# Kernel optimization log

Hardware: AMD Instinct MI355X
Metric: run time of the kernel (lower is better)

## Reference

```python
import jax, jax.numpy as jnp
import numpy as np

B, S, D, H = 2, 2048, 1024, 8
DH = D // H          # hidden_dim == attn_dim == 128
TOTAL = 4 * D        # (2*hidden_dim + 2*attn_dim) * H
EPS = 1e-5
ROPE_BASE = 10000.0


def _layernorm(x, g, b):
    m = jnp.mean(x, axis=-1, keepdims=True)
    v = jnp.mean(jnp.square(x - m), axis=-1, keepdims=True)
    return (x - m) * jax.lax.rsqrt(v + EPS) * g + b


def _rope(x):
    # x: [B, H, S, DH], interleaved even/odd RoPE as in the torch module
    half = DH // 2
    inv_freq = 1.0 / (ROPE_BASE ** (jnp.arange(0, DH, 2, dtype=jnp.float32) / DH))  # [half]
    t = jnp.arange(x.shape[2], dtype=jnp.float32)
    freqs = t[:, None] * inv_freq[None, :]                 # [S, half]
    cos = jnp.cos(freqs)[None, None, :, :]                 # [1,1,S,half]
    sin = jnp.sin(freqs)[None, None, :, :]
    xe, xo = x[..., 0::2], x[..., 1::2]
    re = xe * cos - xo * sin
    ro = xe * sin + xo * cos
    return jnp.stack([re, ro], axis=-1).reshape(x.shape)


def setup_inputs() -> dict:
    key = jax.random.key(0)
    ks = jax.random.split(key, 6)
    x = jax.random.normal(ks[0], (B, S, D), dtype=jnp.float32)
    attention_mask = jnp.ones((B, S), dtype=bool)
    # weights stored [in, out] so forward is x @ W + b
    w_uvqk = 0.02 * jax.random.normal(ks[1], (D, TOTAL), dtype=jnp.float32)
    b_uvqk = jnp.zeros((TOTAL,), dtype=jnp.float32)
    w_out = 0.02 * jax.random.normal(ks[2], (3 * D, D), dtype=jnp.float32)
    b_out = jnp.zeros((D,), dtype=jnp.float32)
    ln1_g = jnp.ones((D,), dtype=jnp.float32)
    ln1_b = jnp.zeros((D,), dtype=jnp.float32)
    ln2_g = jnp.ones((D,), dtype=jnp.float32)
    ln2_b = jnp.zeros((D,), dtype=jnp.float32)
    return {"x": x, "attention_mask": attention_mask,
            "ln1_g": ln1_g, "ln1_b": ln1_b,
            "w_uvqk": w_uvqk, "b_uvqk": b_uvqk,
            "ln2_g": ln2_g, "ln2_b": ln2_b,
            "w_out": w_out, "b_out": b_out}


def reference(x, attention_mask, ln1_g, ln1_b, w_uvqk, b_uvqk, ln2_g, ln2_b, w_out, b_out):
    normed = _layernorm(x, ln1_g, ln1_b)
    uvqk = jax.nn.silu(normed @ w_uvqk + b_uvqk)          # [B,S,4D]
    u, v, q, k = jnp.split(uvqk, [D, 2 * D, 3 * D], axis=-1)
    q = q.reshape(B, S, H, DH).transpose(0, 2, 1, 3)      # [B,H,S,DH]
    k = k.reshape(B, S, H, DH).transpose(0, 2, 1, 3)
    v = v.reshape(B, S, H, DH).transpose(0, 2, 1, 3)
    q, k = _rope(q), _rope(k)
    scale = jnp.float32(DH) ** 0.5
    scores = jnp.einsum('bhsd,bhtd->bhst', q, k) / scale  # [B,H,S,S] fp32
    causal = jnp.tril(jnp.ones((S, S), dtype=bool))
    pad = attention_mask[:, None, :, None] & attention_mask[:, None, None, :]
    valid = pad & causal[None, None, :, :]
    scores = jnp.where(valid, scores, jnp.float32(-30.0))
    scores = jnp.clip(scores, -30.0, 30.0)
    attn = jax.nn.silu(scores)                            # SiLU instead of softmax
    ao = jnp.einsum('bhst,bhtd->bhsd', attn, v)           # [B,H,S,DH]
    ao = ao.transpose(0, 2, 1, 3).reshape(B, S, D)
    normed_attn = _layernorm(ao, ln2_g, ln2_b)
    cat = jnp.concatenate([u, ao, normed_attn * u], axis=-1)  # [B,S,3D]
    return x + (cat @ w_out + b_out)
```

## Files before the change

kernel.cpp:

```cpp
#include <hip/hip_runtime.h>
#include <hip/hip_bf16.h>
#include <math.h>

#define Bm 2
#define Sm 2048
#define Dm 1024
#define Hm 8
#define DHm 128
#define TOTALm 4096
#define ROWS (Bm*Sm)
#define K2m (3*Dm)

typedef __bf16 bf16;
typedef __bf16 bf16x8 __attribute__((ext_vector_type(8)));
typedef __bf16 bf16x4 __attribute__((ext_vector_type(4)));
typedef float  f32x4  __attribute__((ext_vector_type(4)));

__device__ __forceinline__ void stage_tile_128x32(
    const bf16* __restrict__ g, int ld, bf16* lds, int tid)
{
    int wid = tid >> 6;
    #pragma unroll
    for (int j = 0; j < 2; j++) {
        int e0  = (j*256 + tid) * 8;
        int row = e0 >> 5, col = e0 & 31;
        const bf16* src = g + (size_t)row*ld + col;
        bf16* dst = lds + (size_t)(j*256 + wid*64)*8;
        __builtin_amdgcn_global_load_lds(
            (const __attribute__((address_space(1))) unsigned int*)src,
            (__attribute__((address_space(3))) unsigned int*)dst,
            16, 0, 0);
    }
}

__device__ __forceinline__ void stage_tile_64x32(
    const bf16* __restrict__ g, int ld, bf16* lds, int tid)
{
    int wid = tid >> 6;
    int e0 = tid * 8;
    int row = e0 >> 5, col = e0 & 31;
    const bf16* src = g + (size_t)row*ld + col;
    bf16* dst = lds + (size_t)wid*512;
    __builtin_amdgcn_global_load_lds(
        (const __attribute__((address_space(1))) unsigned int*)src,
        (__attribute__((address_space(3))) unsigned int*)dst,
        16, 0, 0);
}

__global__ __launch_bounds__(256) void prep_kernel(
    const float* __restrict__ x, const float* __restrict__ g1,
    const float* __restrict__ b1, bf16* __restrict__ normed,
    const float* __restrict__ w_uvqk, bf16* __restrict__ Wt1,
    const float* __restrict__ w_out,  bf16* __restrict__ Wt2,
    float* __restrict__ ct, float* __restrict__ st)
{
    __shared__ float tile[32][33];
    __shared__ float red[4];
    __shared__ float stats[2];
    int bid = blockIdx.x;
    int tid = threadIdx.x;
    if (bid < 7168) {
        const float* in; bf16* out; int R, C, bx, by;
        if (bid < 4096) { in = w_uvqk; out = Wt1; R = Dm;  C = TOTALm; bx = bid & 127; by = bid >> 7; }
        else { int id2 = bid - 4096; in = w_out; out = Wt2; R = K2m; C = Dm; bx = id2 & 31; by = id2 >> 5; }
        int c0 = bx*32, r0 = by*32;
        int tx = tid & 31, ty = tid >> 5;
        for (int i=0;i<4;i++) {
            int r = ty + i*8;
            tile[r][tx] = in[(size_t)(r0+r)*C + c0+tx];
        }
        __syncthreads();
        for (int i=0;i<4;i++) {
            int cl = ty + i*8;
            out[(size_t)(c0+cl)*R + r0+tx] = (bf16)tile[tx][cl];
        }
    } else if (bid < 7680) {
        int idx = (bid - 7168)*256 + tid;
        int t = idx >> 6, p = idx & 63;
        float inv = expf(-0.143911568f * (float)p);
        float f = (float)t * inv;
        float sv, cv;
        sincosf(f, &sv, &cv);
        ct[idx] = cv; st[idx] = sv;
    } else {
        int row = bid - 7680;
        const float* xr = x + (size_t)row * Dm;
        float4 v = *(const float4*)(xr + tid*4);
        float s = v.x+v.y+v.z+v.w;
        for (int o=32;o>0;o>>=1) s += __shfl_down(s,o);
        int wid = tid>>6, lane = tid&63;
        if (lane==0) red[wid]=s;
        __syncthreads();
        if (tid==0) stats[0] = (red[0]+red[1]+red[2]+red[3]) * (1.f/Dm);
        __syncthreads();
        float m = stats[0];
        float d0=v.x-m,d1=v.y-m,d2=v.z-m,d3=v.w-m;
        float q = d0*d0+d1*d1+d2*d2+d3*d3;
        for (int o=32;o>0;o>>=1) q += __shfl_down(q,o);
        if (lane==0) red[wid]=q;
        __syncthreads();
        if (tid==0) stats[1] = rsqrtf((red[0]+red[1]+red[2]+red[3])*(1.f/Dm) + 1e-5f);
        __syncthreads();
        float rs = stats[1];
        float4 gv = *(const float4*)(g1 + tid*4);
        float4 bv = *(const float4*)(b1 + tid*4);
        bf16x4 o;
        o[0] = (bf16)(d0*rs*gv.x + bv.x);
        o[1] = (bf16)(d1*rs*gv.y + bv.y);
        o[2] = (bf16)(d2*rs*gv.z + bv.z);
        o[3] = (bf16)(d3*rs*gv.w + bv.w);
        *(bf16x4*)(normed + (size_t)row*Dm + tid*4) = o;
    }
}

__global__ __launch_bounds__(256,4) void gemm1_kernel(
    const bf16* __restrict__ A, const bf16* __restrict__ Bt,
    const float* __restrict__ bias,
    const float* __restrict__ ct, const float* __restrict__ st,
    bf16* __restrict__ cat, bf16* __restrict__ qb, bf16* __restrict__ kb,
    bf16* __restrict__ vt)
{
    __shared__ __align__(16) bf16 sm[17408];
    const int K = Dm;
    int m0 = blockIdx.y*128, n0 = blockIdx.x*128;
    int tid = threadIdx.x, wid = tid>>6, lane = tid&63;
    int quad = lane>>4, l16 = lane&15;
    int wm = (wid>>1)*64, wn = (wid&1)*64;
    f32x4 acc[4][4] = {};
    bf16* sA = sm;
    bf16* sB = sm + 8192;
    for (int k0=0;k0<K;k0+=64) {
        __syncthreads();
        stage_tile_128x32(A  + (size_t)m0*K + k0,      K, sA,        tid);
        stage_tile_128x32(A  + (size_t)m0*K + k0 + 32, K, sA + 4096, tid);
        stage_tile_128x32(Bt + (size_t)n0*K + k0,      K, sB,        tid);
        stage_tile_128x32(Bt + (size_t)n0*K + k0 + 32, K, sB + 4096, tid);
        __syncthreads();
        #pragma unroll
        for (int kc=0;kc<2;kc++) {
            bf16x8 af[4], bfr[4];
            #pragma unroll
            for (int t=0;t<4;t++) af[t]  = *(const bf16x8*)&sA[kc*4096 + (wm+t*16+l16)*32 + quad*8];
            #pragma unroll
            for (int t=0;t<4;t++) bfr[t] = *(const bf16x8*)&sB[kc*4096 + (wn+t*16+l16)*32 + quad*8];
            #pragma unroll
            for (int tm=0;tm<4;tm++)
                #pragma unroll
                for (int tn=0;tn<4;tn++)
                    acc[tm][tn] = __builtin_amdgcn_mfma_f32_16x16x32_bf16(af[tm], bfr[tn], acc[tm][tn], 0,0,0);
        }
    }
    int sect = n0 >> 10;
    if (sect == 1) {
        __syncthreads();
        #pragma unroll
        for (int tm=0;tm<4;tm++)
        #pragma unroll
        for (int tn=0;tn<4;tn++) {
            int colg = n0 + wn + tn*16 + l16;
            float bval = bias[colg];
            int d = colg & 127;
            #pragma unroll
            for (int r=0;r<4;r++) {
                int srow = wm + tm*16 + quad*4 + r;
                float val = acc[tm][tn][r] + bval;
                val = val / (1.f + __expf(-val));
                sm[d*136 + srow] = (bf16)val;
            }
        }
        __syncthreads();
        int h = (n0 >> 7) & 7;
        int b = m0 >> 11, s0l = m0 & 2047;
        int d2 = tid >> 1, sh = (tid & 1)*64;
        bf16* dst = vt + ((size_t)(b*Hm+h)*DHm + d2)*Sm + s0l + sh;
        const bf16* srcl = &sm[d2*136 + sh];
        #pragma unroll
        for (int i=0;i<8;i++)
            *(bf16x8*)(dst + i*8) = *(const bf16x8*)(srcl + i*8);
    } else if (sect == 0) {
        #pragma unroll
        for (int tm=0;tm<4;tm++)
        #pragma unroll
        for (int tn=0;tn<4;tn++) {
            int c = n0 + wn + tn*16 + l16;
            float bval = bias[c];
            #pragma unroll
            for (int r=0;r<4;r++) {
                int row = m0 + wm + tm*16 + quad*4 + r;
                float val = acc[tm][tn][r] + bval;
                val = val / (1.f + __expf(-val));
                cat[(size_t)row*K2m + c] = (bf16)val;
            }
        }
    } else {
        bf16* dstb = (sect==2) ? qb : kb;
        float postscale = (sect==2) ? 0.08838834764831845f : 1.0f;
        #pragma unroll
        for (int tm=0;tm<4;tm++)
        #pragma unroll
        for (int tn=0;tn<4;tn++) {
            int colg = n0 + wn + tn*16 + l16;
            int c = colg & 1023;
            int h = c>>7, d = c&127, p = d>>1;
            float bval = bias[colg];
            #pragma unroll
            for (int r=0;r<4;r++) {
                int row = m0 + wm + tm*16 + quad*4 + r;
                float val = acc[tm][tn][r] + bval;
                val = val / (1.f + __expf(-val));
                int b = row>>11, s = row&2047;
                float pv = __shfl_xor(val, 1);
                float cv = ct[s*64+p], sv = st[s*64+p];
                float res = (d&1) ? (pv*sv + val*cv) : (val*cv - pv*sv);
                dstb[((size_t)(b*Hm+h)*Sm + s)*DHm + d] = (bf16)(res * postscale);
            }
        }
    }
}

__global__ __launch_bounds__(256,3) void attn_kernel(
    const bf16* __restrict__ qb, const bf16* __restrict__ kb,
    const bf16* __restrict__ vt, float* __restrict__ ao0,
    float* __restrict__ ao1)
{
    __shared__ __align__(16) bf16 sK[16384];
    __shared__ __align__(16) bf16 P[64*136];
    int bid = blockIdx.x;
    int head = bid & 15;
    int idx = bid >> 4;
    int b = head >> 3, h = head & 7;
    int qt, k_begin, k_end;
    float* aoOut;
    if (idx < 32) {
        qt = 31 - (idx >> 1);
        int nkt = (qt >> 1) + 1;
        int half = (nkt + 1) >> 1;
        if ((idx & 1) == 0) { k_begin = 0;    k_end = half; aoOut = ao0; }
        else                { k_begin = half; k_end = nkt;  aoOut = ao1; }
    } else {
        qt = 47 - idx;
        k_begin = 0; k_end = (qt >> 1) + 1;
        aoOut = ao0;
    }
    const size_t headoff = (size_t)(b*Hm+h)*Sm*DHm;
    const bf16* Q  = qb + headoff;
    const bf16* Km = kb + headoff;
    const bf16* V  = vt + headoff;
    int tid=threadIdx.x, wid=tid>>6, lane=tid&63, quad=lane>>4, l16=lane&15;
    int wm=(wid>>1)*32, wn=(wid&1)*64;
    int q0 = qt*64;
    f32x4 accO[2][4] = {};
    bf16x8 qf[4][2];
    #pragma unroll
    for (int kc=0;kc<4;kc++)
        #pragma unroll
        for (int t=0;t<2;t++)
            qf[kc][t] = *(const bf16x8*)(Q + (size_t)(q0+wm+t*16+l16)*DHm + kc*32 + quad*8);
    int e0 = tid*8, e1 = (256+tid)*8;
    int kr0 = e0>>5, kcol0 = e0&31;
    int kr1 = e1>>5, kcol1 = e1&31;
    bf16x8 kreg[4][2];
    {
        int t0 = k_begin*128;
        #pragma unroll
        for (int kc=0;kc<4;kc++) {
            kreg[kc][0] = *(const bf16x8*)(Km + (size_t)(t0+kr0)*DHm + kc*32 + kcol0);
            kreg[kc][1] = *(const bf16x8*)(Km + (size_t)(t0+kr1)*DHm + kc*32 + kcol1);
        }
    }
    for (int kt=k_begin; kt<k_end; kt++) {
        int t0 = kt*128;
        __syncthreads();
        #pragma unroll
        for (int kc=0;kc<4;kc++) {
            *(bf16x8*)&sK[kc*4096 + e0] = kreg[kc][0];
            *(bf16x8*)&sK[kc*4096 + e1] = kreg[kc][1];
        }
        __syncthreads();
        if (kt+1 < k_end) {
            int t0n = t0 + 128;
            #pragma unroll
            for (int kc=0;kc<4;kc++) {
                kreg[kc][0] = *(const bf16x8*)(Km + (size_t)(t0n+kr0)*DHm + kc*32 + kcol0);
                kreg[kc][1] = *(const bf16x8*)(Km + (size_t)(t0n+kr1)*DHm + kc*32 + kcol1);
            }
        }
        bool clean = (t0 + 127 <= q0);
        #pragma unroll
        for (int ts=0; ts<4; ts++) {
            f32x4 accS[2] = {};
            #pragma unroll
            for (int kc=0;kc<4;kc++) {
                bf16x8 bfr = *(const bf16x8*)&sK[kc*4096 + (wn+ts*16+l16)*32 + quad*8];
                #pragma unroll
                for (int tm=0;tm<2;tm++)
                    accS[tm] = __builtin_amdgcn_mfma_f32_16x16x32_bf16(qf[kc][tm], bfr, accS[tm], 0,0,0);
            }
            #pragma unroll
            for (int tm=0;tm<2;tm++)
                #pragma unroll
                for (int r=0;r<4;r++) {
                    int srow = wm+tm*16+quad*4+r;
                    int tcol = wn+ts*16+l16;
                    float s = fminf(30.f, fmaxf(-30.f, accS[tm][r]));
                    float p = s * __builtin_amdgcn_rcpf(1.f + __expf(-s));
                    if (!clean && (t0+tcol > q0+srow)) p = 0.f;
                    P[srow*136 + tcol] = (bf16)p;
                }
        }
        __syncthreads();
        int kcn = ((q0 + 63 - t0) >> 5) + 1;
        if (kcn > 4) kcn = 4;
        for (int kc=0;kc<kcn;kc++) {
            bf16x8 af[2], bfr[4];
            #pragma unroll
            for (int t=0;t<2;t++) af[t]  = *(const bf16x8*)&P[(wm+t*16+l16)*136 + kc*32 + quad*8];
            #pragma unroll
            for (int t=0;t<4;t++) bfr[t] = *(const bf16x8*)(V + (size_t)(wn+t*16+l16)*Sm + t0 + kc*32 + quad*8);
            #pragma unroll
            for (int tm=0;tm<2;tm++)
                #pragma unroll
                for (int tn=0;tn<4;tn++)
                    accO[tm][tn] = __builtin_amdgcn_mfma_f32_16x16x32_bf16(af[tm], bfr[tn], accO[tm][tn], 0,0,0);
        }
    }
    #pragma unroll
    for (int tm=0;tm<2;tm++)
    #pragma unroll
    for (int tn=0;tn<4;tn++)
        #pragma unroll
        for (int r=0;r<4;r++) {
            int s = q0+wm+tm*16+quad*4+r;
            int d = wn+tn*16+l16;
            aoOut[((size_t)(b*Sm+s))*Dm + h*DHm + d] = accO[tm][tn][r];
        }
}

__global__ __launch_bounds__(256) void ln2_cat_kernel(
    const float* __restrict__ ao0, const float* __restrict__ ao1,
    const float* __restrict__ g,
    const float* __restrict__ bb, bf16* __restrict__ cat)
{
    int row = blockIdx.x;
    int tid = threadIdx.x;
    float4 v  = *(const float4*)(ao0 + (size_t)row*Dm + tid*4);
    float4 v1 = *(const float4*)(ao1 + (size_t)row*Dm + tid*4);
    v.x += v1.x; v.y += v1.y; v.z += v1.z; v.w += v1.w;
    float s = v.x+v.y+v.z+v.w;
    for (int o=32;o>0;o>>=1) s += __shfl_down(s,o);
    __shared__ float red[4]; __shared__ float stats[2];
    int wid = tid>>6, lane = tid&63;
    if (lane==0) red[wid]=s;
    __syncthreads();
    if (tid==0) stats[0] = (red[0]+red[1]+red[2]+red[3]) * (1.f/Dm);
    __syncthreads();
    float m = stats[0];
    float d0=v.x-m,d1=v.y-m,d2=v.z-m,d3=v.w-m;
    float q = d0*d0+d1*d1+d2*d2+d3*d3;
    for (int o=32;o>0;o>>=1) q += __shfl_down(q,o);
    if (lane==0) red[wid]=q;
    __syncthreads();
    if (tid==0) stats[1] = rsqrtf((red[0]+red[1]+red[2]+red[3])*(1.f/Dm) + 1e-5f);
    __syncthreads();
    float rs = stats[1];
    float4 gv = *(const float4*)(g + tid*4);
    float4 bv = *(const float4*)(bb + tid*4);
    bf16* crow = cat + (size_t)row * K2m;
    bf16x4 u4 = *(const bf16x4*)(crow + tid*4);
    bf16x4 a4, nu4;
    a4[0]=(bf16)v.x; a4[1]=(bf16)v.y; a4[2]=(bf16)v.z; a4[3]=(bf16)v.w;
    nu4[0]=(bf16)(((v.x-m)*rs*gv.x+bv.x) * (float)u4[0]);
    nu4[1]=(bf16)(((v.y-m)*rs*gv.y+bv.y) * (float)u4[1]);
    nu4[2]=(bf16)(((v.z-m)*rs*gv.z+bv.z) * (float)u4[2]);
    nu4[3]=(bf16)(((v.w-m)*rs*gv.w+bv.w) * (float)u4[3]);
    *(bf16x4*)(crow + 1024 + tid*4) = a4;
    *(bf16x4*)(crow + 2048 + tid*4) = nu4;
}

__global__ __launch_bounds__(256,4) void gemm2_kernel(
    const bf16* __restrict__ A, const bf16* __restrict__ Bt,
    const float* __restrict__ bias, const float* __restrict__ x,
    float* __restrict__ out)
{
    __shared__ __align__(16) bf16 sm[12288];
    const int K = K2m, N = Dm;
    int m0 = blockIdx.y*128, n0 = blockIdx.x*64;
    int tid = threadIdx.x, wid = tid>>6, lane = tid&63;
    int quad = lane>>4, l16 = lane&15;
    int wm = (wid>>1)*64, wn = (wid&1)*32;
    f32x4 acc[4][2] = {};
    bf16* sA = sm;
    bf16* sB = sm + 8192;
    for (int k0=0;k0<K;k0+=64) {
        __syncthreads();
        stage_tile_128x32(A  + (size_t)m0*K + k0,      K, sA,        tid);
        stage_tile_128x32(A  + (size_t)m0*K + k0 + 32, K, sA + 4096, tid);
        stage_tile_64x32 (Bt + (size_t)n0*K + k0,      K, sB,        tid);
        stage_tile_64x32 (Bt + (size_t)n0*K + k0 + 32, K, sB + 2048, tid);
        __syncthreads();
        #pragma unroll
        for (int kc=0;kc<2;kc++) {
            bf16x8 af[4], bfr[2];
            #pragma unroll
            for (int t=0;t<4;t++) af[t]  = *(const bf16x8*)&sA[kc*4096 + (wm+t*16+l16)*32 + quad*8];
            #pragma unroll
            for (int t=0;t<2;t++) bfr[t] = *(const bf16x8*)&sB[kc*2048 + (wn+t*16+l16)*32 + quad*8];
            #pragma unroll
            for (int tm=0;tm<4;tm++)
                #pragma unroll
                for (int tn=0;tn<2;tn++)
                    acc[tm][tn] = __builtin_amdgcn_mfma_f32_16x16x32_bf16(af[tm], bfr[tn], acc[tm][tn], 0,0,0);
        }
    }
    #pragma unroll
    for (int tm=0;tm<4;tm++)
    #pragma unroll
    for (int tn=0;tn<2;tn++) {
        int col = n0 + wn + tn*16 + l16;
        float bval = bias[col];
        #pragma unroll
        for (int r=0;r<4;r++) {
            int row = m0 + wm + tm*16 + quad*4 + r;
            out[(size_t)row*N + col] = acc[tm][tn][r] + bval + x[(size_t)row*N + col];
        }
    }
}

extern "C" void kernel_launch(void* const* d_in, const int* in_sizes, int n_in,
                              void* d_out, int out_size, void* d_ws, size_t ws_size,
                              hipStream_t stream)
{
    const float* x      = (const float*)d_in[0];
    const float* ln1_g  = (const float*)d_in[2];
    const float* ln1_b  = (const float*)d_in[3];
    const float* w_uvqk = (const float*)d_in[4];
    const float* b_uvqk = (const float*)d_in[5];
    const float* ln2_g  = (const float*)d_in[6];
    const float* ln2_b  = (const float*)d_in[7];
    const float* w_out  = (const float*)d_in[8];
    const float* b_out  = (const float*)d_in[9];

    char* w = (char*)d_ws;
    bf16*  normed = (bf16*)(w);
    bf16*  Wt1    = (bf16*)(w + 8388608);
    bf16*  Wt2    = (bf16*)(w + 16777216);
    bf16*  qb     = (bf16*)(w + 23068672);
    bf16*  kb     = (bf16*)(w + 31457280);
    bf16*  vt     = (bf16*)(w + 39845888);
    float* ao0    = (float*)(w + 48234496);
    bf16*  cat    = (bf16*)(w + 65011712);
    float* ct     = (float*)(w + 90177536);
    float* st     = (float*)(w + 90701824);
    float* ao1    = (float*)(w);

    prep_kernel<<<11776, 256, 0, stream>>>(x, ln1_g, ln1_b, normed,
                                           w_uvqk, Wt1, w_out, Wt2, ct, st);
    gemm1_kernel<<<dim3(TOTALm/128, ROWS/128), 256, 0, stream>>>(
        normed, Wt1, b_uvqk, ct, st, cat, qb, kb, vt);
    hipMemsetAsync(ao1, 0, (size_t)ROWS*Dm*sizeof(float), stream);
    attn_kernel<<<768, 256, 0, stream>>>(qb, kb, vt, ao0, ao1);
    ln2_cat_kernel<<<ROWS, 256, 0, stream>>>(ao0, ao1, ln2_g, ln2_b, cat);
    gemm2_kernel<<<dim3(Dm/64, ROWS/128), 256, 0, stream>>>(
        cat, Wt2, b_out, x, (float*)d_out);
}
```

Before: 269.4 us.

## Keep attention probabilities in registers via transposed S^T MFMA layout

Attention now computes the transposed score tile (K as the A operand, Q as B), so each lane holds one query row's probabilities in exactly the layout needed as the B operand of a 16x16x16 MFMA for P·V. This removes the LDS P buffer, its stores and reloads, and one __syncthreads per key tile. Each wave now owns 16 full query rows across all 128 head dims, skips fully masked 16-column subtiles, and writes output with float4 stores. The trade-off is smaller-K MFMAs for P·V, more V global loads per wave since every wave reads all of V, and higher register pressure.

```diff
diff --git a/kernel.cpp b/kernel.cpp
--- a/kernel.cpp
+++ b/kernel.cpp
@@ -15,6 +15,17 @@
 typedef __bf16 bf16x8 __attribute__((ext_vector_type(8)));
 typedef __bf16 bf16x4 __attribute__((ext_vector_type(4)));
 typedef float  f32x4  __attribute__((ext_vector_type(4)));
+typedef short  s16x4  __attribute__((ext_vector_type(4)));
+
+__device__ __forceinline__ f32x4 mfma_16x16x16_bf16(bf16x4 a, bf16x4 b, f32x4 c)
+{
+#if __has_builtin(__builtin_amdgcn_mfma_f32_16x16x16_bf16)
+    return __builtin_amdgcn_mfma_f32_16x16x16_bf16(a, b, c, 0, 0, 0);
+#else
+    return __builtin_amdgcn_mfma_f32_16x16x16bf16_1k(
+        __builtin_bit_cast(s16x4, a), __builtin_bit_cast(s16x4, b), c, 0, 0, 0);
+#endif
+}
 
 __device__ __forceinline__ void stage_tile_128x32(
     const bf16* __restrict__ g, int ld, bf16* lds, int tid)
@@ -224,7 +235,6 @@
     float* __restrict__ ao1)
 {
     __shared__ __align__(16) bf16 sK[16384];
-    __shared__ __align__(16) bf16 P[64*136];
     int bid = blockIdx.x;
     int head = bid & 15;
     int idx = bid >> 4;
@@ -247,15 +257,13 @@
     const bf16* Km = kb + headoff;
     const bf16* V  = vt + headoff;
     int tid=threadIdx.x, wid=tid>>6, lane=tid&63, quad=lane>>4, l16=lane&15;
-    int wm=(wid>>1)*32, wn=(wid&1)*64;
     int q0 = qt*64;
-    f32x4 accO[2][4] = {};
-    bf16x8 qf[4][2];
+    int sg = q0 + wid*16 + l16;
+    f32x4 accO[8] = {};
+    bf16x8 qf[4];
     #pragma unroll
     for (int kc=0;kc<4;kc++)
-        #pragma unroll
-        for (int t=0;t<2;t++)
-            qf[kc][t] = *(const bf16x8*)(Q + (size_t)(q0+wm+t*16+l16)*DHm + kc*32 + quad*8);
+        qf[kc] = *(const bf16x8*)(Q + (size_t)sg*DHm + kc*32 + quad*8);
     int e0 = tid*8, e1 = (256+tid)*8;
     int kr0 = e0>>5, kcol0 = e0&31;
     int kr1 = e1>>5, kcol1 = e1&31;
@@ -285,55 +293,47 @@
                 kreg[kc][1] = *(const bf16x8*)(Km + (size_t)(t0n+kr1)*DHm + kc*32 + kcol1);
             }
         }
+        int ttn = ((q0 + 63 - t0) >> 4) + 1;
+        if (ttn > 8) ttn = 8;
         bool clean = (t0 + 127 <= q0);
-        #pragma unroll
-        for (int ts=0; ts<4; ts++) {
-            f32x4 accS[2] = {};
+        bf16x4 pb[8];
+        #pragma unroll
+        for (int tt=0; tt<8; tt++) {
+            if (tt >= ttn) break;
+            f32x4 aS = {};
             #pragma unroll
             for (int kc=0;kc<4;kc++) {
-                bf16x8 bfr = *(const bf16x8*)&sK[kc*4096 + (wn+ts*16+l16)*32 + quad*8];
-                #pragma unroll
-                for (int tm=0;tm<2;tm++)
-                    accS[tm] = __builtin_amdgcn_mfma_f32_16x16x32_bf16(qf[kc][tm], bfr, accS[tm], 0,0,0);
-            }
-            #pragma unroll
-            for (int tm=0;tm<2;tm++)
-                #pragma unroll
-                for (int r=0;r<4;r++) {
-                    int srow = wm+tm*16+quad*4+r;
-                    int tcol = wn+ts*16+l16;
-                    float s = fminf(30.f, fmaxf(-30.f, accS[tm][r]));
-                    float p = s * __builtin_amdgcn_rcpf(1.f + __expf(-s));
-                    if (!clean && (t0+tcol > q0+srow)) p = 0.f;
-                    P[srow*136 + tcol] = (bf16)p;
+                bf16x8 kf = *(const bf16x8*)&sK[kc*4096 + (tt*16+l16)*32 + quad*8];
+                aS = __builtin_amdgcn_mfma_f32_16x16x32_bf16(kf, qf[kc], aS, 0,0,0);
+            }
+            #pragma unroll
+            for (int rr=0; rr<4; rr++) {
+                float s = fminf(30.f, fmaxf(-30.f, aS[rr]));
+                float p = s * __builtin_amdgcn_rcpf(1.f + __expf(-s));
+                if (!clean) {
+                    int tg = t0 + tt*16 + quad*4 + rr;
+                    if (tg > sg) p = 0.f;
                 }
-        }
-        __syncthreads();
-        int kcn = ((q0 + 63 - t0) >> 5) + 1;
-        if (kcn > 4) kcn = 4;
-        for (int kc=0;kc<kcn;kc++) {
-            bf16x8 af[2], bfr[4];
-            #pragma unroll
-            for (int t=0;t<2;t++) af[t]  = *(const bf16x8*)&P[(wm+t*16+l16)*136 + kc*32 + quad*8];
-            #pragma unroll
-            for (int t=0;t<4;t++) bfr[t] = *(const bf16x8*)(V + (size_t)(wn+t*16+l16)*Sm + t0 + kc*32 + quad*8);
-            #pragma unroll
-            for (int tm=0;tm<2;tm++)
-                #pragma unroll
-                for (int tn=0;tn<4;tn++)
-                    accO[tm][tn] = __builtin_amdgcn_mfma_f32_16x16x32_bf16(af[tm], bfr[tn], accO[tm][tn], 0,0,0);
+                pb[tt][rr] = (bf16)p;
+            }
+        }
+        #pragma unroll
+        for (int tt=0; tt<8; tt++) {
+            if (tt >= ttn) break;
+            bf16x4 vf[8];
+            #pragma unroll
+            for (int dt=0; dt<8; dt++)
+                vf[dt] = *(const bf16x4*)(V + (size_t)(dt*16+l16)*Sm + t0 + tt*16 + quad*4);
+            #pragma unroll
+            for (int dt=0; dt<8; dt++)
+                accO[dt] = mfma_16x16x16_bf16(vf[dt], pb[tt], accO[dt]);
         }
     }
     #pragma unroll
-    for (int tm=0;tm<2;tm++)
-    #pragma unroll
-    for (int tn=0;tn<4;tn++)
-        #pragma unroll
-        for (int r=0;r<4;r++) {
-            int s = q0+wm+tm*16+quad*4+r;
-            int d = wn+tn*16+l16;
-            aoOut[((size_t)(b*Sm+s))*Dm + h*DHm + d] = accO[tm][tn][r];
-        }
+    for (int dt=0; dt<8; dt++) {
+        float* dst = aoOut + ((size_t)(b*Sm + sg))*Dm + h*DHm + dt*16 + quad*4;
+        *(float4*)dst = *(float4*)&accO[dt];
+    }
 }
 
 __global__ __launch_bounds__(256) void ln2_cat_kernel(
```

Result: slower. 377.6 us (+40.2%).
